# Kernel optimization log

Hardware: AMD Instinct MI355X
Metric: run time of the kernel (lower is better)

The kernel has to match this reference:

```python
import jax, jax.numpy as jnp
import numpy as np

IN_DIM = 256
QK_DIM = IN_DIM // 8


def setup_inputs() -> dict:
    key = jax.random.key(0)
    ks = jax.random.split(key, 10)
    B, C, W, H = 4, IN_DIM, 64, 64
    a = jax.random.normal(ks[0], (B, C, W, H), dtype=jnp.float32)
    b = jax.random.normal(ks[1], (B, C, W, H), dtype=jnp.float32)
    c = jax.random.uniform(ks[2], (B, 1, 2 * W, 2 * H), dtype=jnp.float32)
    scale = 0.02
    wq = jax.random.normal(ks[3], (QK_DIM, C), dtype=jnp.float32) * scale
    bq = jnp.zeros((QK_DIM,), dtype=jnp.float32)
    wk = jax.random.normal(ks[4], (QK_DIM, C), dtype=jnp.float32) * scale
    bk = jnp.zeros((QK_DIM,), dtype=jnp.float32)
    wv = jax.random.normal(ks[5], (C, C), dtype=jnp.float32) * scale
    bv = jnp.zeros((C,), dtype=jnp.float32)
    gamma = jnp.ones((1,), dtype=jnp.float32)
    return {"a": a, "b": b, "c": c, "wq": wq, "bq": bq, "wk": wk,
            "bk": bk, "wv": wv, "bv": bv, "gamma": gamma}


def reference(a, b, c, wq, bq, wk, bk, wv, bv, gamma):
    B, C, W, H = a.shape
    N = W * H
    # F.interpolate(c, scale_factor=1/down_rate, mode='nearest'): output idx i -> input idx i*down_rate
    down = c.shape[2] // W
    cd = c[:, :, ::down, ::down]                      # [B,1,W,H]
    # 1x1 convs as channel contractions
    q = jnp.einsum('bchw,oc->bohw', a, wq) + bq[None, :, None, None]
    k = jnp.einsum('bchw,oc->bohw', b, wk) + bk[None, :, None, None]
    v = jnp.einsum('bchw,oc->bohw', a, wv) + bv[None, :, None, None]
    qf = q.reshape(B, QK_DIM, N)                      # proj_query^T rows are spatial
    kf = k.reshape(B, QK_DIM, N)
    vf = v.reshape(B, C, N)
    sim = jnp.einsum('bdi,bdj->bij', qf, kf)          # [B,N,N]
    cflat = cd.reshape(B, N)
    # mask[b,i,j] = cflat[b,i] (per-query multiplicative logit scaling)
    logits = sim * cflat[:, :, None]
    attn = jax.nn.softmax(logits, axis=-1)            # [B,N,N]
    out_attn = jnp.einsum('bcj,bij->bci', vf, attn).reshape(B, C, W, H)
    out = gamma * a * cd + (1.0 - cd) * out_attn
    return out
```

## Files before the change

### kernel.cpp

```cpp
#include <hip/hip_runtime.h>

#define LOG2E 1.44269504088896340736f

typedef __attribute__((ext_vector_type(8))) short short8;
typedef __attribute__((ext_vector_type(4))) float float4v;
typedef __attribute__((ext_vector_type(2))) float float2v;
typedef __attribute__((ext_vector_type(2))) int int2v;

__device__ inline unsigned short f2bf(float f) {
    union { float f; unsigned u; } v; v.f = f;
    unsigned r = v.u + 0x7fffu + ((v.u >> 16) & 1u);
    return (unsigned short)(r >> 16);
}
__device__ inline float bf2f(unsigned short u) {
    union { unsigned u; float f; } v; v.u = ((unsigned)u) << 16;
    return v.f;
}
__device__ inline unsigned pk_bf16(float a, float b) {
    union { float f; unsigned u; } ua, ub; ua.f = a; ub.f = b;
    return __builtin_amdgcn_perm(ub.u + 0x8000u, ua.u + 0x8000u, 0x07060302u);
}

__global__ void wcvt_kernel(const float* __restrict__ wq, const float* __restrict__ wk,
                            const float* __restrict__ wv, unsigned short* __restrict__ Wbf)
{
    int idx = blockIdx.x * 256 + threadIdx.x;
    int e4  = idx * 4;
    int row = e4 >> 8, col = e4 & 255;
    const float* src = (row < 32) ? (wq + row * 256 + col)
                     : (row < 64) ? (wk + (row - 32) * 256 + col)
                                  : (wv + (row - 64) * 256 + col);
    float4v v = *(const float4v*)src;
    int2v p;
    p.x = (unsigned)f2bf(v[0]) | ((unsigned)f2bf(v[1]) << 16);
    p.y = (unsigned)f2bf(v[2]) | ((unsigned)f2bf(v[3]) << 16);
    *(int2v*)(Wbf + e4) = p;
}

__launch_bounds__(256, 3)
__global__ void proj_kernel(const float* __restrict__ a_p, const float* __restrict__ b_p,
                            const float* __restrict__ c_p,
                            const float* __restrict__ bq, const float* __restrict__ bk,
                            const float* __restrict__ bv,
                            const unsigned short* __restrict__ Wbf,
                            unsigned short* __restrict__ Qg, unsigned short* __restrict__ Kg,
                            unsigned short* __restrict__ Vg)
{
    __shared__ unsigned At[16 * 132];
    __shared__ unsigned Bt[16 * 132];

    const int t    = threadIdx.x;
    const int blk  = blockIdx.x;
    const int b    = blk & 3;
    const int t16  = blk >> 2;
    const int i0   = t16 * 16;
    const int lane = t & 63;
    const int w    = t >> 6;
    const int q    = lane >> 4;
    const int n    = lane & 15;

    {
        int arr = t >> 7, p = t & 127;
        const float* src = (arr ? b_p : a_p) + ((size_t)(b * 256 + 2 * p)) * 4096 + i0;
        unsigned* dst = arr ? Bt : At;
        float4v r0[4], r1[4];
#pragma unroll
        for (int j4 = 0; j4 < 4; ++j4) r0[j4] = *(const float4v*)(src + j4 * 4);
#pragma unroll
        for (int j4 = 0; j4 < 4; ++j4) r1[j4] = *(const float4v*)(src + 4096 + j4 * 4);
#pragma unroll
        for (int j4 = 0; j4 < 4; ++j4)
#pragma unroll
            for (int jj = 0; jj < 4; ++jj) {
                int i = j4 * 4 + jj;
                dst[i * 132 + p] = (unsigned)f2bf(r0[j4][jj]) | ((unsigned)f2bf(r1[j4][jj]) << 16);
            }
    }
    __syncthreads();

    float4v acc[5];
#pragma unroll
    for (int kk = 0; kk < 5; ++kk) acc[kk] = (float4v){0.f, 0.f, 0.f, 0.f};

#pragma unroll
    for (int kc = 0; kc < 8; ++kc) {
        short8 atf = *(const short8*)((const unsigned short*)At + n * 264 + kc * 32 + q * 8);
        short8 btf = atf;
        if (w >= 2)
            btf = *(const short8*)((const unsigned short*)Bt + n * 264 + kc * 32 + q * 8);
#pragma unroll
        for (int kk = 0; kk < 5; ++kk) {
            int mt = w + 4 * kk;
            short8 wf = *(const short8*)(Wbf + (size_t)(mt * 16 + n) * 256 + kc * 32 + q * 8);
            short8 bsel = (mt == 2 || mt == 3) ? btf : atf;
            acc[kk] = __builtin_amdgcn_mfma_f32_16x16x32_bf16(wf, bsel, acc[kk], 0, 0, 0);
        }
    }

    const int i = i0 + n;
    const int jj = i & 31;
    const int pperm = ((jj & 15) >> 2) * 8 + (jj >> 4) * 4 + (jj & 3);
    const float cdq = c_p[b * 16384 + (i >> 6) * 256 + (i & 63) * 2] * LOG2E;
#pragma unroll
    for (int kk = 0; kk < 5; ++kk) {
        int mt = w + 4 * kk;
#pragma unroll
        for (int r = 0; r < 4; ++r) {
            int mm = mt * 16 + q * 4 + r;
            float bias = (mm < 32) ? bq[mm] : (mm < 64) ? bk[mm - 32] : bv[mm - 64];
            float val = acc[kk][r] + bias;
            if (mm < 32) {
                Qg[(size_t)(b * 4096 + i) * 32 + mm] = f2bf(val * cdq);
            } else if (mm < 64) {
                Kg[(size_t)(b * 4096 + i) * 32 + (mm - 32)] = f2bf(val);
            } else {
                Vg[(size_t)(((b * 128 + (i >> 5)) * 256) + (mm - 64)) * 32 + pperm] = f2bf(val);
            }
        }
    }
}

__launch_bounds__(256, 3)
__global__ void attn_kernel(const unsigned short* __restrict__ Qg,
                            const unsigned short* __restrict__ Kg,
                            const unsigned short* __restrict__ Vg,
                            unsigned short* __restrict__ Opart, float* __restrict__ lsum)
{
    const int t    = threadIdx.x;
    const int blk  = blockIdx.x;
    const int b    = blk & 3;
    const int rt   = (blk >> 2) & 63;
    const int s    = blk >> 8;
    const int i0   = rt * 64;
    const int lane = t & 63;
    const int w    = t >> 6;
    const int q    = lane >> 4;
    const int n    = lane & 15;

    short8 qf[4];
#pragma unroll
    for (int ig = 0; ig < 4; ++ig)
        qf[ig] = *(const short8*)(Qg + (size_t)(b * 4096 + i0 + ig * 16 + n) * 32 + q * 8);

    float4v acc[4][4];
#pragma unroll
    for (int ig = 0; ig < 4; ++ig)
#pragma unroll
        for (int ct = 0; ct < 4; ++ct) acc[ig][ct] = (float4v){0.f, 0.f, 0.f, 0.f};
    float lsc[4] = {0.f, 0.f, 0.f, 0.f};

    const float4v m16v = (float4v){-16.f, -16.f, -16.f, -16.f};

    const unsigned short* kb = Kg + (size_t)(b * 4096 + s * 1024 + n) * 32 + q * 8;
    const unsigned short* vb = Vg + ((size_t)((b * 128 + s * 32) * 256 + w * 64 + n)) * 32 + q * 8;

    short8 kf0 = *(const short8*)(kb);
    short8 kf1 = *(const short8*)(kb + 512);

#pragma unroll 1
    for (int it = 0; it < 32; ++it) {
        short8 vf[4];
#pragma unroll
        for (int ct = 0; ct < 4; ++ct)
            vf[ct] = *(const short8*)(vb + ct * 512);

        short8 pf[4];
#pragma unroll
        for (int ig = 0; ig < 4; ++ig) {
            float4v s0 = __builtin_amdgcn_mfma_f32_16x16x32_bf16(kf0, qf[ig], m16v, 0, 0, 0);
            float4v s1 = __builtin_amdgcn_mfma_f32_16x16x32_bf16(kf1, qf[ig], m16v, 0, 0, 0);
            float p0 = __builtin_amdgcn_exp2f(s0[0]), p1 = __builtin_amdgcn_exp2f(s0[1]);
            float p2 = __builtin_amdgcn_exp2f(s0[2]), p3 = __builtin_amdgcn_exp2f(s0[3]);
            float p4 = __builtin_amdgcn_exp2f(s1[0]), p5 = __builtin_amdgcn_exp2f(s1[1]);
            float p6 = __builtin_amdgcn_exp2f(s1[2]), p7 = __builtin_amdgcn_exp2f(s1[3]);
            lsc[ig] += ((p0 + p1) + (p2 + p3)) + ((p4 + p5) + (p6 + p7));
            union { short8 s8; unsigned u[4]; } pf_;
            pf_.u[0] = pk_bf16(p0, p1);
            pf_.u[1] = pk_bf16(p2, p3);
            pf_.u[2] = pk_bf16(p4, p5);
            pf_.u[3] = pk_bf16(p6, p7);
            pf[ig] = pf_.s8;
        }

        kf0 = *(const short8*)(kb + 1024);
        kf1 = *(const short8*)(kb + 1536);

#pragma unroll
        for (int ig = 0; ig < 4; ++ig)
#pragma unroll
            for (int ct = 0; ct < 4; ++ct)
                acc[ig][ct] = __builtin_amdgcn_mfma_f32_16x16x32_bf16(pf[ig], vf[ct], acc[ig][ct], 0, 0, 0);

        kb += 1024;
        vb += 8192;
    }

    const size_t obase = (size_t)blk * 16384;
#pragma unroll
    for (int ig = 0; ig < 4; ++ig)
#pragma unroll
        for (int ct = 0; ct < 4; ++ct) {
            int c = w * 64 + ct * 16 + n;
            int i = ig * 16 + q * 4;
            int2v pk;
            pk.x = (int)pk_bf16(acc[ig][ct][0], acc[ig][ct][1]);
            pk.y = (int)pk_bf16(acc[ig][ct][2], acc[ig][ct][3]);
            *(int2v*)(Opart + obase + (size_t)c * 64 + i) = pk;
        }
#pragma unroll
    for (int ig = 0; ig < 4; ++ig) {
        float v = lsc[ig];
        v += __shfl_xor(v, 16, 64);
        v += __shfl_xor(v, 32, 64);
        if (w == 0 && lane < 16)
            lsum[(size_t)blk * 64 + ig * 16 + lane] = v;
    }
}

__launch_bounds__(256, 4)
__global__ void combine_kernel(const float* __restrict__ a_p, const float* __restrict__ c_p,
                               const float* __restrict__ gamma_p,
                               const unsigned short* __restrict__ Opart,
                               const float* __restrict__ lsum, float* __restrict__ out)
{
    __shared__ float invL[64];
    __shared__ float cdl[64];

    const int t   = threadIdx.x;
    const int blk = blockIdx.x;
    const int b   = blk & 3;
    const int rt  = (blk >> 2) & 63;
    const int cs  = blk >> 8;
    const int i0  = rt * 64;

    if (t < 64) {
        float L = 0.f;
#pragma unroll
        for (int s = 0; s < 4; ++s)
            L += lsum[(size_t)((s << 8) | (rt << 2) | b) * 64 + t];
        invL[t] = 1.0f / L;
        cdl[t] = c_p[b * 16384 + rt * 256 + 2 * t];
    }
    __syncthreads();

    const float gam = gamma_p[0];
    const int il = (t & 31) * 2;
    const int cq = t >> 5;
#pragma unroll
    for (int k = 0; k < 4; ++k) {
        int c = cs * 32 + cq + 8 * k;
        float o0 = 0.f, o1 = 0.f;
#pragma unroll
        for (int s = 0; s < 4; ++s) {
            int idx = (s << 8) | (rt << 2) | b;
            unsigned pr = *(const unsigned*)(Opart + (size_t)idx * 16384 + (size_t)c * 64 + il);
            o0 += bf2f((unsigned short)(pr & 0xffff));
            o1 += bf2f((unsigned short)(pr >> 16));
        }
        o0 *= invL[il];
        o1 *= invL[il + 1];
        size_t gi = (size_t)(b * 256 + c) * 4096 + i0 + il;
        float2v av = *(const float2v*)(a_p + gi);
        float cd0 = cdl[il], cd1 = cdl[il + 1];
        float2v ov;
        ov[0] = gam * av[0] * cd0 + (1.0f - cd0) * o0;
        ov[1] = gam * av[1] * cd1 + (1.0f - cd1) * o1;
        *(float2v*)(out + gi) = ov;
    }
}

extern "C" void kernel_launch(void* const* d_in, const int* in_sizes, int n_in,
                              void* d_out, int out_size, void* d_ws, size_t ws_size,
                              hipStream_t stream)
{
    const float* a_p   = (const float*)d_in[0];
    const float* b_p   = (const float*)d_in[1];
    const float* c_p   = (const float*)d_in[2];
    const float* wq    = (const float*)d_in[3];
    const float* bq    = (const float*)d_in[4];
    const float* wk    = (const float*)d_in[5];
    const float* bk    = (const float*)d_in[6];
    const float* wv    = (const float*)d_in[7];
    const float* bv    = (const float*)d_in[8];
    const float* gamma = (const float*)d_in[9];
    float* out = (float*)d_out;

    unsigned short* Qg    = (unsigned short*)d_ws;
    unsigned short* Kg    = Qg + (size_t)4 * 4096 * 32;
    unsigned short* Vg    = Kg + (size_t)4 * 4096 * 32;
    unsigned short* Wbf   = Vg + (size_t)4 * 256 * 4096;
    unsigned short* Opart = Wbf + (size_t)320 * 256;
    float*          lsum  = (float*)(Opart + (size_t)1024 * 16384);

    wcvt_kernel<<<80, 256, 0, stream>>>(wq, wk, wv, Wbf);
    proj_kernel<<<1024, 256, 0, stream>>>(a_p, b_p, c_p, bq, bk, bv, Wbf, Qg, Kg, Vg);
    attn_kernel<<<1024, 256, 0, stream>>>(Qg, Kg, Vg, Opart, lsum);
    combine_kernel<<<2048, 256, 0, stream>>>(a_p, c_p, gamma, Opart, lsum, out);
}
```

Measured before the change: 195.4 us.

## Restructure projection staging, remap attention block order, use nontemporal partial stores

The projection kernel now stages its input in two halves to lower register pressure, and its k-loop is only partially unrolled. The attention kernel reorders block indices so that adjacent blocks share split pairs, which may improve cache locality on K/V. A logical index keeps the output layout unchanged. Partial outputs are written with nontemporal 64-bit stores so they do not pollute the cache. These are several small unrelated tweaks, and the reduced unroll could cost some instruction-level parallelism.

Measured after the change: 197.2 us. No clear change (+1.0%).

```diff
diff --git a/kernel.cpp b/kernel.cpp
--- a/kernel.cpp
+++ b/kernel.cpp
@@ -62,19 +62,20 @@
     {
         int arr = t >> 7, p = t & 127;
         const float* src = (arr ? b_p : a_p) + ((size_t)(b * 256 + 2 * p)) * 4096 + i0;
-        unsigned* dst = arr ? Bt : At;
-        float4v r0[4], r1[4];
-#pragma unroll
-        for (int j4 = 0; j4 < 4; ++j4) r0[j4] = *(const float4v*)(src + j4 * 4);
-#pragma unroll
-        for (int j4 = 0; j4 < 4; ++j4) r1[j4] = *(const float4v*)(src + 4096 + j4 * 4);
-#pragma unroll
-        for (int j4 = 0; j4 < 4; ++j4)
-#pragma unroll
-            for (int jj = 0; jj < 4; ++jj) {
-                int i = j4 * 4 + jj;
-                dst[i * 132 + p] = (unsigned)f2bf(r0[j4][jj]) | ((unsigned)f2bf(r1[j4][jj]) << 16);
-            }
+        unsigned* dst = (arr ? Bt : At) + p;
+#pragma unroll
+        for (int h = 0; h < 2; ++h) {
+            float4v r0a = *(const float4v*)(src + h * 8);
+            float4v r0b = *(const float4v*)(src + h * 8 + 4);
+            float4v r1a = *(const float4v*)(src + 4096 + h * 8);
+            float4v r1b = *(const float4v*)(src + 4096 + h * 8 + 4);
+#pragma unroll
+            for (int jj = 0; jj < 4; ++jj)
+                dst[(h * 8 + jj) * 132] = (unsigned)f2bf(r0a[jj]) | ((unsigned)f2bf(r1a[jj]) << 16);
+#pragma unroll
+            for (int jj = 0; jj < 4; ++jj)
+                dst[(h * 8 + 4 + jj) * 132] = (unsigned)f2bf(r0b[jj]) | ((unsigned)f2bf(r1b[jj]) << 16);
+        }
     }
     __syncthreads();
 
@@ -82,7 +83,7 @@
 #pragma unroll
     for (int kk = 0; kk < 5; ++kk) acc[kk] = (float4v){0.f, 0.f, 0.f, 0.f};
 
-#pragma unroll
+#pragma unroll 2
     for (int kc = 0; kc < 8; ++kc) {
         short8 atf = *(const short8*)((const unsigned short*)At + n * 264 + kc * 32 + q * 8);
         short8 btf = atf;
@@ -129,8 +130,10 @@
     const int t    = threadIdx.x;
     const int blk  = blockIdx.x;
     const int b    = blk & 3;
-    const int rt   = (blk >> 2) & 63;
-    const int s    = blk >> 8;
+    const int s_lo = (blk >> 2) & 1;
+    const int rt   = (blk >> 3) & 63;
+    const int s    = s_lo + 2 * (blk >> 9);
+    const int lidx = (s << 8) | (rt << 2) | b;
     const int i0   = rt * 64;
     const int lane = t & 63;
     const int w    = t >> 6;
@@ -195,17 +198,18 @@
         vb += 8192;
     }
 
-    const size_t obase = (size_t)blk * 16384;
+    const size_t obase = (size_t)lidx * 16384;
 #pragma unroll
     for (int ig = 0; ig < 4; ++ig)
 #pragma unroll
         for (int ct = 0; ct < 4; ++ct) {
             int c = w * 64 + ct * 16 + n;
             int i = ig * 16 + q * 4;
-            int2v pk;
-            pk.x = (int)pk_bf16(acc[ig][ct][0], acc[ig][ct][1]);
-            pk.y = (int)pk_bf16(acc[ig][ct][2], acc[ig][ct][3]);
-            *(int2v*)(Opart + obase + (size_t)c * 64 + i) = pk;
+            unsigned long long pk =
+                (unsigned long long)pk_bf16(acc[ig][ct][0], acc[ig][ct][1]) |
+                ((unsigned long long)pk_bf16(acc[ig][ct][2], acc[ig][ct][3]) << 32);
+            __builtin_nontemporal_store(pk,
+                (unsigned long long*)(Opart + obase + (size_t)c * 64 + i));
         }
 #pragma unroll
     for (int ig = 0; ig < 4; ++ig) {
@@ -213,7 +217,7 @@
         v += __shfl_xor(v, 16, 64);
         v += __shfl_xor(v, 32, 64);
         if (w == 0 && lane < 16)
-            lsum[(size_t)blk * 64 + ig * 16 + lane] = v;
+            lsum[(size_t)lidx * 64 + ig * 16 + lane] = v;
     }
 }
 
```
